# Optimization experiments

Hardware: AMD Instinct MI355X
Metric: run time of the kernel (lower is better)

## Reference

```python
import jax, jax.numpy as jnp
import numpy as np

B, D, C = 16384, 2048, 1000  # batch, in_features (feature dim), out_features (classes)
INIT_SCALE = 10.0
EPS = 1e-12


def setup_inputs() -> dict:
    key = jax.random.key(0)
    k1, k2 = jax.random.split(key)
    x = jax.random.normal(k1, (B, D), dtype=jnp.float32)
    weights = jax.random.normal(k2, (C, D), dtype=jnp.float32)  # prototypes
    scales = jnp.ones((1,), dtype=jnp.float32) * INIT_SCALE
    return {"x": x, "weights": weights, "scales": scales}


def reference(x, weights, scales):
    # Pairwise Euclidean distance between features [B,D] and prototypes [C,D]
    x2 = jnp.sum(x * x, axis=-1, keepdims=True)            # [B,1]
    w2 = jnp.sum(weights * weights, axis=-1)               # [C]
    cross = jnp.einsum('bd,cd->bc', x, weights)            # [B,C]
    d2 = jnp.maximum(x2 + w2[None, :] - 2.0 * cross, EPS)  # clamp for sqrt stability
    distances = jnp.sqrt(d2)                               # [B,C]
    logits = -scales * distances  # dml forward: -self.learn(distances)
    return logits
```

## Files before the change

### kernel.cpp

```cpp
#include <hip/hip_runtime.h>
#include <hip/hip_bf16.h>
#include <stdint.h>

#define B_ROWS 16384
#define D_K    2048
#define C_COLS 1000
#define C_PAD  1024
#define EPS_D2 1e-12f

#define BM 256
#define BN 128
#define BK 32
#define NT (D_K / BK)
#define BUFB 24576
#define NBUF 3

typedef __attribute__((ext_vector_type(8))) short bf16x8;
typedef __attribute__((ext_vector_type(4))) float f32x4;

__device__ __forceinline__ void async16(void* lds, const void* g) {
    __builtin_amdgcn_global_load_lds(
        (const __attribute__((address_space(1))) unsigned int*)g,
        (__attribute__((address_space(3))) unsigned int*)lds,
        16, 0, 0);
}

__device__ __forceinline__ uint2 pack_bf16x4(float4 v) {
    union { __hip_bfloat162 h; uint32_t u; } a, b;
    a.h = __float22bfloat162_rn(make_float2(v.x, v.y));
    b.h = __float22bfloat162_rn(make_float2(v.z, v.w));
    uint2 r; r.x = a.u; r.y = b.u; return r;
}

__global__ __launch_bounds__(256) void prep_all(
    const float* __restrict__ x, const float* __restrict__ w,
    __hip_bfloat16* __restrict__ xb, __hip_bfloat16* __restrict__ wb,
    float* __restrict__ x2, float* __restrict__ w2) {
    const int t = threadIdx.x;
    const int wave = t >> 6;
    const int lane = t & 63;
    const int row = blockIdx.x * 4 + wave;

    const float* src;
    uint4* dst;
    float* norm_out;
    bool valid;
    if (row < B_ROWS) {
        src = x + (size_t)row * D_K;
        dst = (uint4*)(xb + (size_t)row * D_K);
        norm_out = x2 + row;
        valid = true;
    } else {
        int c = row - B_ROWS;
        src = w + (size_t)c * D_K;
        dst = (uint4*)(wb + (size_t)c * D_K);
        norm_out = w2 + c;
        valid = (c < C_COLS);
    }

    float4 v[8];
    if (valid) {
        const float4* s4 = (const float4*)src;
        #pragma unroll
        for (int i = 0; i < 4; i++) {
            v[2 * i]     = s4[2 * lane + 128 * i];
            v[2 * i + 1] = s4[2 * lane + 1 + 128 * i];
        }
    } else {
        #pragma unroll
        for (int i = 0; i < 8; i++) v[i] = make_float4(0.f, 0.f, 0.f, 0.f);
    }

    float ss = 0.f;
    #pragma unroll
    for (int i = 0; i < 8; i++)
        ss += v[i].x * v[i].x + v[i].y * v[i].y + v[i].z * v[i].z + v[i].w * v[i].w;

    #pragma unroll
    for (int i = 0; i < 4; i++) {
        uint2 a = pack_bf16x4(v[2 * i]);
        uint2 b = pack_bf16x4(v[2 * i + 1]);
        uint4 p; p.x = a.x; p.y = a.y; p.z = b.x; p.w = b.y;
        dst[lane + 64 * i] = p;
    }

    #pragma unroll
    for (int off = 32; off > 0; off >>= 1) ss += __shfl_down(ss, off, 64);
    if (lane == 0 && valid) *norm_out = ss;
}

__global__ __launch_bounds__(512, 4) void dml_gemm(
    const __hip_bfloat16* __restrict__ A,
    const __hip_bfloat16* __restrict__ Bm,
    const float* __restrict__ x2, const float* __restrict__ w2,
    const float* __restrict__ scales, float* __restrict__ out)
{
    __shared__ __align__(16) char smem[NBUF * BUFB];

    const int tid  = threadIdx.x;
    const int wave = tid >> 6;
    const int lane = tid & 63;
    const int wm = wave >> 1;
    const int wn = wave & 1;

    const int id  = blockIdx.x;
    const int xcd = id & 7;
    const int j5  = id >> 3;
    const int m0  = (xcd * 8 + (j5 & 7)) * BM;
    const int n0  = (j5 >> 3) * BN;

    const int L0 = tid, L1 = tid + 512;
    const int r0 = L0 >> 2, g0 = (L0 & 3) ^ ((r0 >> 1) & 3);
    const int r1 = L1 >> 2, g1 = (L1 & 3) ^ ((r1 >> 1) & 3);
    const int rB = tid >> 2, gB = (tid & 3) ^ ((rB >> 1) & 3);
    const __hip_bfloat16* pA0 = A  + (size_t)(m0 + r0) * D_K + g0 * 8;
    const __hip_bfloat16* pA1 = A  + (size_t)(m0 + r1) * D_K + g1 * 8;
    const __hip_bfloat16* pB  = Bm + (size_t)(n0 + rB) * D_K + gB * 8;
    char* ldA0 = smem + L0 * 16;
    char* ldA1 = smem + L1 * 16;
    char* ldB  = smem + 16384 + tid * 16;

    const int fr  = lane & 15;
    const int fq  = lane >> 4;
    const int fsw = (fr >> 1) & 3;
    const char* fA = smem + (wm * 64 + fr) * 64 + (fq ^ fsw) * 16;
    const char* fB = smem + 16384 + (wn * 64 + fr) * 64 + (fq ^ fsw) * 16;

    f32x4 acc[4][4] = {};

    async16(ldA0,        pA0);      async16(ldA1,        pA1);      async16(ldB,        pB);
    async16(ldA0 + BUFB, pA0 + 32); async16(ldA1 + BUFB, pA1 + 32); async16(ldB + BUFB, pB + 32);
    asm volatile("s_waitcnt vmcnt(3)" ::: "memory");
    __builtin_amdgcn_s_barrier();
    __builtin_amdgcn_sched_barrier(0);

    int bo = 0, sbo = 2 * BUFB;
    #pragma unroll 1
    for (int t = 0; t < NT; ++t) {
        if (t + 2 < NT) {
            async16(ldA0 + sbo, pA0 + (t + 2) * BK);
            async16(ldA1 + sbo, pA1 + (t + 2) * BK);
            async16(ldB  + sbo, pB  + (t + 2) * BK);
        }

        bf16x8 b[4], a[4];
        #pragma unroll
        for (int q = 0; q < 4; ++q) b[q] = *(const bf16x8*)(fB + bo + q * 1024);
        #pragma unroll
        for (int i = 0; i < 4; ++i) a[i] = *(const bf16x8*)(fA + bo + i * 1024);
        __builtin_amdgcn_s_setprio(1);
        #pragma unroll
        for (int i = 0; i < 4; ++i)
            #pragma unroll
            for (int q = 0; q < 4; ++q)
                acc[i][q] = __builtin_amdgcn_mfma_f32_16x16x32_bf16(a[i], b[q], acc[i][q], 0, 0, 0);
        __builtin_amdgcn_s_setprio(0);

        if (t < NT - 2)       asm volatile("s_waitcnt vmcnt(3)" ::: "memory");
        else if (t == NT - 2) asm volatile("s_waitcnt vmcnt(0)" ::: "memory");
        if (t < NT - 1) {
            __builtin_amdgcn_s_barrier();
            __builtin_amdgcn_sched_barrier(0);
        }
        bo  = (bo  == 2 * BUFB) ? 0 : bo  + BUFB;
        sbo = (sbo == 2 * BUFB) ? 0 : sbo + BUFB;
    }

    const float s = scales[0];
    const int colb = n0 + wn * 64 + fr;
    const int rowb = m0 + wm * 64 + fq * 4;

    float w2v[4];
    #pragma unroll
    for (int q = 0; q < 4; ++q) w2v[q] = w2[colb + q * 16];

    #pragma unroll
    for (int i = 0; i < 4; ++i) {
        float x2v[4];
        #pragma unroll
        for (int r = 0; r < 4; ++r) x2v[r] = x2[rowb + i * 16 + r];
        #pragma unroll
        for (int q = 0; q < 4; ++q) {
            if (colb + q * 16 < C_COLS) {
                float* orow = out + (size_t)(rowb + i * 16) * C_COLS + colb + q * 16;
                #pragma unroll
                for (int r = 0; r < 4; ++r) {
                    float d2 = x2v[r] + w2v[q] - 2.0f * acc[i][q][r];
                    d2 = fmaxf(d2, EPS_D2);
                    orow[(size_t)r * C_COLS] = -s * __builtin_sqrtf(d2);
                }
            }
        }
    }
}

extern "C" void kernel_launch(void* const* d_in, const int* in_sizes, int n_in,
                              void* d_out, int out_size, void* d_ws, size_t ws_size,
                              hipStream_t stream) {
    const float* x      = (const float*)d_in[0];
    const float* w      = (const float*)d_in[1];
    const float* scales = (const float*)d_in[2];
    float* out = (float*)d_out;

    char* ws = (char*)d_ws;
    __hip_bfloat16* xb = (__hip_bfloat16*)ws;
    __hip_bfloat16* wb = (__hip_bfloat16*)(ws + (size_t)B_ROWS * D_K * 2);
    float* x2 = (float*)(ws + (size_t)B_ROWS * D_K * 2 + (size_t)C_PAD * D_K * 2);
    float* w2 = x2 + B_ROWS;

    prep_all<<<dim3((B_ROWS + C_PAD) / 4), dim3(256), 0, stream>>>(x, w, xb, wb, x2, w2);
    dml_gemm<<<dim3((B_ROWS / BM) * (C_PAD / BN)), dim3(512), 0, stream>>>(xb, wb, x2, w2, scales, out);
}
```

Before: 297.9 us.

## Fuse bf16 prep into GEMM kernel with atomic-flag grid synchronization

Merges the fp32-to-bf16 conversion and norm computation into the GEMM kernel. Each of the 512 blocks converts 32 x rows and 2 weight rows, then signals atomic counters, and spins until its A-panel group and all weight rows are ready. Non-temporal loads and stores are used for the x stream. This removes the second kernel launch and the tail gap between kernels, at the cost of a memset, spin-waiting, and a reliance on all 512 blocks being co-resident to avoid deadlock.

Result: slower. 419.4 us (+40.8%).

```diff
diff --git a/kernel.cpp b/kernel.cpp
--- a/kernel.cpp
+++ b/kernel.cpp
@@ -17,6 +17,8 @@
 
 typedef __attribute__((ext_vector_type(8))) short bf16x8;
 typedef __attribute__((ext_vector_type(4))) float f32x4;
+typedef __attribute__((ext_vector_type(4))) float f4;
+typedef __attribute__((ext_vector_type(4))) unsigned u4;
 
 __device__ __forceinline__ void async16(void* lds, const void* g) {
     __builtin_amdgcn_global_load_lds(
@@ -25,89 +27,105 @@
         16, 0, 0);
 }
 
-__device__ __forceinline__ uint2 pack_bf16x4(float4 v) {
-    union { __hip_bfloat162 h; uint32_t u; } a, b;
-    a.h = __float22bfloat162_rn(make_float2(v.x, v.y));
-    b.h = __float22bfloat162_rn(make_float2(v.z, v.w));
-    uint2 r; r.x = a.u; r.y = b.u; return r;
-}
-
-__global__ __launch_bounds__(256) void prep_all(
-    const float* __restrict__ x, const float* __restrict__ w,
-    __hip_bfloat16* __restrict__ xb, __hip_bfloat16* __restrict__ wb,
-    float* __restrict__ x2, float* __restrict__ w2) {
-    const int t = threadIdx.x;
-    const int wave = t >> 6;
-    const int lane = t & 63;
-    const int row = blockIdx.x * 4 + wave;
-
-    const float* src;
-    uint4* dst;
-    float* norm_out;
-    bool valid;
-    if (row < B_ROWS) {
-        src = x + (size_t)row * D_K;
-        dst = (uint4*)(xb + (size_t)row * D_K);
-        norm_out = x2 + row;
-        valid = true;
+__device__ __forceinline__ unsigned pack2(float a, float b) {
+    union { __hip_bfloat162 h; unsigned u; } r;
+    r.h = __float22bfloat162_rn(make_float2(a, b));
+    return r.u;
+}
+
+template<bool NTH>
+__device__ __forceinline__ void prep_row(const float* src, __hip_bfloat16* dstp,
+                                         float* norm_out, int lane, bool valid) {
+    const f4* s4 = (const f4*)src;
+    u4* dst = (u4*)dstp;
+    f4 v[8];
+    if (valid) {
+        #pragma unroll
+        for (int i = 0; i < 4; i++) {
+            if (NTH) {
+                v[2 * i]     = __builtin_nontemporal_load(&s4[2 * lane + 128 * i]);
+                v[2 * i + 1] = __builtin_nontemporal_load(&s4[2 * lane + 1 + 128 * i]);
+            } else {
+                v[2 * i]     = s4[2 * lane + 128 * i];
+                v[2 * i + 1] = s4[2 * lane + 1 + 128 * i];
+            }
+        }
     } else {
-        int c = row - B_ROWS;
-        src = w + (size_t)c * D_K;
-        dst = (uint4*)(wb + (size_t)c * D_K);
-        norm_out = w2 + c;
-        valid = (c < C_COLS);
-    }
-
-    float4 v[8];
-    if (valid) {
-        const float4* s4 = (const float4*)src;
-        #pragma unroll
-        for (int i = 0; i < 4; i++) {
-            v[2 * i]     = s4[2 * lane + 128 * i];
-            v[2 * i + 1] = s4[2 * lane + 1 + 128 * i];
-        }
-    } else {
-        #pragma unroll
-        for (int i = 0; i < 8; i++) v[i] = make_float4(0.f, 0.f, 0.f, 0.f);
-    }
-
+        #pragma unroll
+        for (int i = 0; i < 8; i++) v[i] = (f4)0.f;
+    }
     float ss = 0.f;
     #pragma unroll
     for (int i = 0; i < 8; i++)
         ss += v[i].x * v[i].x + v[i].y * v[i].y + v[i].z * v[i].z + v[i].w * v[i].w;
-
     #pragma unroll
     for (int i = 0; i < 4; i++) {
-        uint2 a = pack_bf16x4(v[2 * i]);
-        uint2 b = pack_bf16x4(v[2 * i + 1]);
-        uint4 p; p.x = a.x; p.y = a.y; p.z = b.x; p.w = b.y;
-        dst[lane + 64 * i] = p;
-    }
-
+        u4 p;
+        p.x = pack2(v[2 * i].x,     v[2 * i].y);
+        p.y = pack2(v[2 * i].z,     v[2 * i].w);
+        p.z = pack2(v[2 * i + 1].x, v[2 * i + 1].y);
+        p.w = pack2(v[2 * i + 1].z, v[2 * i + 1].w);
+        if (NTH) __builtin_nontemporal_store(p, &dst[lane + 64 * i]);
+        else     dst[lane + 64 * i] = p;
+    }
     #pragma unroll
     for (int off = 32; off > 0; off >>= 1) ss += __shfl_down(ss, off, 64);
     if (lane == 0 && valid) *norm_out = ss;
 }
 
-__global__ __launch_bounds__(512, 4) void dml_gemm(
-    const __hip_bfloat16* __restrict__ A,
-    const __hip_bfloat16* __restrict__ Bm,
-    const float* __restrict__ x2, const float* __restrict__ w2,
-    const float* __restrict__ scales, float* __restrict__ out)
+__global__ __launch_bounds__(512, 4) void dml_fused(
+    const float* __restrict__ X, const float* __restrict__ W,
+    const float* __restrict__ scales,
+    __hip_bfloat16* __restrict__ xb, __hip_bfloat16* __restrict__ wb,
+    float* __restrict__ x2, float* __restrict__ w2,
+    unsigned* __restrict__ flags,
+    float* __restrict__ out)
 {
     __shared__ __align__(16) char smem[NBUF * BUFB];
 
     const int tid  = threadIdx.x;
     const int wave = tid >> 6;
     const int lane = tid & 63;
-    const int wm = wave >> 1;
-    const int wn = wave & 1;
-
-    const int id  = blockIdx.x;
+    const int id   = blockIdx.x;
+
+    #pragma unroll 1
+    for (int rr = 0; rr < 4; ++rr) {
+        const int row = id * 32 + wave * 4 + rr;
+        prep_row<true>(X + (size_t)row * D_K, xb + (size_t)row * D_K,
+                       x2 + row, lane, true);
+    }
+    if (wave < 2) {
+        const int c = id * 2 + wave;
+        prep_row<false>(W + (size_t)c * D_K, wb + (size_t)c * D_K,
+                        w2 + c, lane, c < C_COLS);
+    }
+    __syncthreads();
+    if (tid == 0) {
+        __threadfence();
+        __hip_atomic_fetch_add(&flags[id >> 3], 1u, __ATOMIC_RELEASE, __HIP_MEMORY_SCOPE_AGENT);
+        __hip_atomic_fetch_add(&flags[64],      1u, __ATOMIC_RELEASE, __HIP_MEMORY_SCOPE_AGENT);
+    }
+
     const int xcd = id & 7;
     const int j5  = id >> 3;
     const int m0  = (xcd * 8 + (j5 & 7)) * BM;
     const int n0  = (j5 >> 3) * BN;
+    const int pm  = xcd * 8 + (j5 & 7);
+
+    if (tid == 0) {
+        while (__hip_atomic_load(&flags[pm], __ATOMIC_ACQUIRE, __HIP_MEMORY_SCOPE_AGENT) < 8u)
+            __builtin_amdgcn_s_sleep(2);
+        while (__hip_atomic_load(&flags[64], __ATOMIC_ACQUIRE, __HIP_MEMORY_SCOPE_AGENT) < 512u)
+            __builtin_amdgcn_s_sleep(2);
+        __threadfence();
+    }
+    __syncthreads();
+
+    const int wm = wave >> 1;
+    const int wn = wave & 1;
+
+    const __hip_bfloat16* A  = xb;
+    const __hip_bfloat16* Bm = wb;
 
     const int L0 = tid, L1 = tid + 512;
     const int r0 = L0 >> 2, g0 = (L0 & 3) ^ ((r0 >> 1) & 3);
@@ -204,10 +222,11 @@
 
     char* ws = (char*)d_ws;
     __hip_bfloat16* xb = (__hip_bfloat16*)ws;
-    __hip_bfloat16* wb = (__hip_bfloat16*)(ws + (size_t)B_ROWS * D_K * 2);
-    float* x2 = (float*)(ws + (size_t)B_ROWS * D_K * 2 + (size_t)C_PAD * D_K * 2);
-    float* w2 = x2 + B_ROWS;
-
-    prep_all<<<dim3((B_ROWS + C_PAD) / 4), dim3(256), 0, stream>>>(x, w, xb, wb, x2, w2);
-    dml_gemm<<<dim3((B_ROWS / BM) * (C_PAD / BN)), dim3(512), 0, stream>>>(xb, wb, x2, w2, scales, out);
-}
+    __hip_bfloat16* wb = (__hip_bfloat16*)(ws + 67108864ull);
+    float* x2 = (float*)(ws + 71303168ull);
+    float* w2 = (float*)(ws + 71368704ull);
+    unsigned* flags = (unsigned*)(ws + 71372800ull);
+
+    hipMemsetAsync(flags, 0, 65 * sizeof(unsigned), stream);
+    dml_fused<<<dim3(512), dim3(512), 0, stream>>>(x, w, scales, xb, wb, x2, w2, flags, out);
+}
```
